# Optimization experiments

Hardware: AMD Instinct MI355X
Metric: run time of the kernel (lower is better)

The kernel has to match this reference:

```python
import jax, jax.numpy as jnp
import numpy as np

B, S, D, H = 16, 2048, 1024, 1024

def setup_inputs() -> dict:
    key = jax.random.key(0)
    k1, k2, k3 = jax.random.split(key, 3)
    X = jax.random.normal(k1, (B, S, D), dtype=jnp.float32)
    W = jax.random.normal(k2, (3 * H, D), dtype=jnp.float32) * (1.0 / np.sqrt(D))
    b = jax.random.normal(k3, (3 * H,), dtype=jnp.float32) * 0.01
    return {"X": X, "W": W, "b": b}

def forget_mult(z, f):
    # z, f: [B, S, H]; h_t = z_t * f_t + (1 - f_t) * h_{t-1}, h_{-1} = 0
    z_t = jnp.moveaxis(z, 1, 0)  # [S, B, H]
    f_t = jnp.moveaxis(f, 1, 0)
    h0 = jnp.zeros(z.shape[::2], dtype=z.dtype)  # [B, H]
    def step(h, zf):
        zt, ft = zf
        h = zt * ft + (1.0 - ft) * h
        return h, h
    _, cs = jax.lax.scan(step, h0, (z_t, f_t))
    return jnp.moveaxis(cs, 0, 1)  # [B, S, H]

def reference(X, W, b):
    # window=1, output_gate=True, batch_first=True, zoneout=0, hidden=None
    Y = jnp.einsum('bsd,ed->bse', X, W) + b  # [B, S, 3H]
    z_gate, f_gate, o_gate = jnp.split(Y, 3, axis=2)
    z_gate = jnp.tanh(z_gate)
    f_gate = jax.nn.sigmoid(f_gate)
    c_gate = forget_mult(z_gate, f_gate)
    output = jax.nn.sigmoid(o_gate) * c_gate
    return output, c_gate[:, -1:]
```

## Files before the change

kernel.cpp:

```cpp
#include <hip/hip_runtime.h>
#include <hip/hip_bf16.h>
#include <hip/hip_fp16.h>


#define BB 16
#define SS 2048
#define DD 1024
#define HH 1024
#define N3 3072
#define CHUNK 64
#define NC (SS/CHUNK)

#define BM 256
#define BN 256
#define BK 64
#define NKT (DD/BK)

typedef _Float16 f16x8 __attribute__((ext_vector_type(8)));
typedef float    f32x4 __attribute__((ext_vector_type(4)));

__device__ __forceinline__ float sigm_f(float x) {
    return 1.0f / (1.0f + __expf(-x));
}
__device__ __forceinline__ float tanh_f(float x) {
    float ax = fabsf(x);
    float e  = __expf(2.0f * ax);
    float r  = 1.0f - 2.0f / (e + 1.0f);
    return copysignf(r, x);
}

__global__ __launch_bounds__(256) void cvt_f32_f16(
    const float* __restrict__ src, __half* __restrict__ dst, int n8)
{
    int i = blockIdx.x * 256 + threadIdx.x;
    if (i >= n8) return;
    const float4* s = (const float4*)src + (size_t)i * 2;
    float4 a = s[0], b = s[1];
    f16x8 v;
    v[0] = (_Float16)a.x; v[1] = (_Float16)a.y; v[2] = (_Float16)a.z; v[3] = (_Float16)a.w;
    v[4] = (_Float16)b.x; v[5] = (_Float16)b.y; v[6] = (_Float16)b.z; v[7] = (_Float16)b.w;
    *((f16x8*)dst + i) = v;
}

__global__ __launch_bounds__(512) void gemm_gates8(
    const __half* __restrict__ Xs,
    const __half* __restrict__ W16,
    const float*  __restrict__ bias,
    __half* __restrict__ G)
{
    __shared__ __half As[2][BM * BK] __attribute__((aligned(16)));
    __shared__ __half Bs[2][BN * BK] __attribute__((aligned(16)));

    const int t   = threadIdx.x;
    const int wid = t >> 6;
    const int l   = t & 63;
    const int m0  = blockIdx.x * BM;
    const int n0  = blockIdx.y * BN;
    const int wr  = wid >> 2;
    const int wc  = wid & 3;
    const int cl  = l & 15;
    const int kg  = l >> 4;
    const int cs  = cl & 7;

    f32x4 acc[8][4];
    #pragma unroll
    for (int m = 0; m < 8; ++m)
        #pragma unroll
        for (int n = 0; n < 4; ++n)
            acc[m][n] = f32x4{0.f, 0.f, 0.f, 0.f};

    const int srow = wid * 8 + (l >> 3);
    const int scol = (((l & 7) ^ ((l >> 3) & 7)) * 8);
    const __half* Xb = Xs  + (size_t)(m0 + srow) * DD + scol;
    const __half* Wb = W16 + (size_t)(n0 + srow) * DD + scol;

#define ISSUE_A(slot, j, kt) \
    __builtin_amdgcn_global_load_lds( \
        (const __attribute__((address_space(1))) void*)(Xb + (size_t)(j) * 64 * DD + (kt) * BK), \
        (__attribute__((address_space(3))) void*)(&As[slot][(j) * 4096 + wid * 512]), 16, 0, 0)
#define ISSUE_B(slot, j, kt) \
    __builtin_amdgcn_global_load_lds( \
        (const __attribute__((address_space(1))) void*)(Wb + (size_t)(j) * 64 * DD + (kt) * BK), \
        (__attribute__((address_space(3))) void*)(&Bs[slot][(j) * 4096 + wid * 512]), 16, 0, 0)

#define READ_A(rh) \
    _Pragma("unroll") \
    for (int i = 0; i < 4; ++i) \
        _Pragma("unroll") \
        for (int kh = 0; kh < 2; ++kh) \
            a[i][kh] = *(const f16x8*)(Ab + ((wr * 128 + ((rh) * 4 + i) * 16 + cl) * BK \
                                             + (((kh * 4 + kg) ^ cs) * 8)))
#define READ_B(bd, ch) \
    _Pragma("unroll") \
    for (int j = 0; j < 2; ++j) \
        _Pragma("unroll") \
        for (int kh = 0; kh < 2; ++kh) \
            bd[j][kh] = *(const f16x8*)(Bb + ((wc * 64 + ((ch) * 2 + j) * 16 + cl) * BK \
                                              + (((kh * 4 + kg) ^ cs) * 8)))

#define WAIT_MFMA(rh, ch, bd) \
    asm volatile("s_waitcnt lgkmcnt(0)" ::: "memory"); \
    __builtin_amdgcn_sched_barrier(0); \
    __builtin_amdgcn_s_setprio(1); \
    _Pragma("unroll") \
    for (int kh = 0; kh < 2; ++kh) \
        _Pragma("unroll") \
        for (int i = 0; i < 4; ++i) \
            _Pragma("unroll") \
            for (int j = 0; j < 2; ++j) \
                acc[(rh) * 4 + i][(ch) * 2 + j] = __builtin_amdgcn_mfma_f32_16x16x32_f16( \
                    a[i][kh], bd[j][kh], acc[(rh) * 4 + i][(ch) * 2 + j], 0, 0, 0); \
    __builtin_amdgcn_s_setprio(0)

    ISSUE_A(0, 0, 0); ISSUE_A(0, 1, 0); ISSUE_A(0, 2, 0); ISSUE_A(0, 3, 0);
    ISSUE_B(0, 0, 0); ISSUE_B(0, 1, 0); ISSUE_B(0, 2, 0); ISSUE_B(0, 3, 0);

    for (int kt = 0; kt < NKT; ++kt) {
        const int cur = kt & 1, nxt = cur ^ 1;
        const __half* Ab = As[cur];
        const __half* Bb = Bs[cur];

        if (kt + 1 < NKT) {
            ISSUE_A(nxt, 0, kt + 1); ISSUE_A(nxt, 1, kt + 1);
            ISSUE_A(nxt, 2, kt + 1); ISSUE_A(nxt, 3, kt + 1);
            asm volatile("s_waitcnt vmcnt(4)" ::: "memory");
        } else {
            asm volatile("s_waitcnt vmcnt(0)" ::: "memory");
        }
        __builtin_amdgcn_s_barrier();

        f16x8 a[4][2], b0[2][2], b1[2][2];

        READ_A(0); READ_B(b0, 0);
        WAIT_MFMA(0, 0, b0);

        READ_B(b1, 1);
        if (kt + 1 < NKT) {
            ISSUE_B(nxt, 0, kt + 1); ISSUE_B(nxt, 1, kt + 1);
            ISSUE_B(nxt, 2, kt + 1); ISSUE_B(nxt, 3, kt + 1);
        }
        WAIT_MFMA(0, 1, b1);

        READ_A(1);
        WAIT_MFMA(1, 1, b1);

        WAIT_MFMA(1, 0, b0);

        __builtin_amdgcn_s_barrier();
    }
#undef WAIT_MFMA
#undef READ_A
#undef READ_B
#undef ISSUE_A
#undef ISSUE_B

    __half* sh = &As[0][0];
    const int bcol0 = n0 + wc * 64 + cl;
    float bv[4];
    #pragma unroll
    for (int fc = 0; fc < 4; ++fc) bv[fc] = bias[bcol0 + fc * 16];

    const int row_l = t >> 3;
    const int chunk = t & 7;

    #pragma unroll
    for (int r = 0; r < 4; ++r) {
        if (wr == (r >> 1)) {
            #pragma unroll
            for (int f4 = 0; f4 < 4; ++f4) {
                const int fr = (r & 1) * 4 + f4;
                #pragma unroll
                for (int fc = 0; fc < 4; ++fc) {
                    #pragma unroll
                    for (int i = 0; i < 4; ++i) {
                        sh[(f4 * 16 + kg * 4 + i) * 264 + wc * 64 + fc * 16 + cl] =
                            __float2half(acc[fr][fc][i] + bv[fc]);
                    }
                }
            }
        }
        __builtin_amdgcn_s_barrier();
        {
            const __half* src = sh + row_l * 264 + chunk * 32;
            __half* dst = G + (size_t)(m0 + r * 64 + row_l) * N3 + n0 + chunk * 32;
            #pragma unroll
            for (int k = 0; k < 4; ++k)
                *(f16x8*)(dst + k * 8) = *(const f16x8*)(src + k * 8);
        }
        __builtin_amdgcn_s_barrier();
    }
}

__global__ __launch_bounds__(256) void scan_pass1(
    const __half* __restrict__ G,
    float* __restrict__ Ac, float* __restrict__ Fc)
{
    const int flat = blockIdx.x * 256 + threadIdx.x;
    const int h  = flat & (HH - 1);
    const int c  = (flat >> 10) & (NC - 1);
    const int lb = flat >> 15;

    const __half* g = G + (size_t)(lb * SS + c * CHUNK) * N3 + h;
    float A = 0.f, F = 1.f;
    for (int s = 0; s < CHUNK; ++s) {
        float z = __half2float(g[0]);
        float f = __half2float(g[HH]);
        g += N3;
        float ft = sigm_f(f);
        float fp = 1.f - ft;
        A = tanh_f(z) * ft + fp * A;
        F *= fp;
    }
    Ac[flat] = A;
    Fc[flat] = F;
}

__global__ __launch_bounds__(256) void scan_pass2(
    const float* __restrict__ Ac, const float* __restrict__ Fc,
    float* __restrict__ Hin, float* __restrict__ c_last)
{
    const int flat = blockIdx.x * 256 + threadIdx.x;
    const int lb = flat >> 10;
    const int h  = flat & (HH - 1);
    float hc = 0.f;
    for (int c = 0; c < NC; ++c) {
        const size_t idx = (size_t)(lb * NC + c) * HH + h;
        Hin[idx] = hc;
        hc = Ac[idx] + Fc[idx] * hc;
    }
    c_last[flat] = hc;
}

__global__ __launch_bounds__(256) void scan_pass3(
    const __half* __restrict__ G, const float* __restrict__ Hin,
    float* __restrict__ out)
{
    const int flat = blockIdx.x * 256 + threadIdx.x;
    const int h  = flat & (HH - 1);
    const int c  = (flat >> 10) & (NC - 1);
    const int lb = flat >> 15;

    const __half* g = G + (size_t)(lb * SS + c * CHUNK) * N3 + h;
    float* o = out + (size_t)(lb * SS + c * CHUNK) * HH + h;
    float hc = Hin[flat];
    for (int s = 0; s < CHUNK; ++s) {
        float z  = __half2float(g[0]);
        float f  = __half2float(g[HH]);
        float og = __half2float(g[2 * HH]);
        g += N3;
        float ft = sigm_f(f);
        hc = tanh_f(z) * ft + (1.f - ft) * hc;
        *o = hc * sigm_f(og);
        o += HH;
    }
}

extern "C" void kernel_launch(void* const* d_in, const int* in_sizes, int n_in,
                              void* d_out, int out_size, void* d_ws, size_t ws_size,
                              hipStream_t stream) {
    const float* X    = (const float*)d_in[0];
    const float* W    = (const float*)d_in[1];
    const float* bias = (const float*)d_in[2];
    for (int i = 0; i < n_in && i < 3; ++i) {
        if      (in_sizes[i] == BB * SS * DD) X    = (const float*)d_in[i];
        else if (in_sizes[i] == N3 * DD)      W    = (const float*)d_in[i];
        else if (in_sizes[i] == N3)           bias = (const float*)d_in[i];
    }
    float* out = (float*)d_out;
    float* c_last_base = out + (size_t)BB * SS * HH;

    const size_t w16_b   = (size_t)N3 * DD * sizeof(__half);
    const size_t per_b_x = (size_t)SS * DD * sizeof(__half);
    const size_t per_b_g = (size_t)SS * N3 * sizeof(__half);
    const size_t per_b_s = (size_t)NC * HH * sizeof(float) * 3;
    int nb = 1;
    for (int cand = BB; cand >= 1; --cand) {
        if (w16_b + (size_t)cand * (per_b_x + per_b_g + per_b_s) <= ws_size) {
            nb = cand; break;
        }
    }
    if (nb > 8) nb = 8;

    __half* W16 = (__half*)d_ws;
    __half* X16 = (__half*)((char*)W16 + w16_b);
    __half* G   = (__half*)((char*)X16 + (size_t)nb * per_b_x);
    float*  Ac  = (float*)((char*)G + (size_t)nb * per_b_g);
    float*  Fc  = Ac + (size_t)nb * NC * HH;
    float*  Hin = Fc + (size_t)nb * NC * HH;

    {
        const int n8 = (N3 * DD) / 8;
        cvt_f32_f16<<<(n8 + 255) / 256, 256, 0, stream>>>(W, W16, n8);
    }

    for (int b0 = 0; b0 < BB; b0 += nb) {
        const int bs = (b0 + nb <= BB) ? nb : (BB - b0);

        const int n8x = (bs * SS * DD) / 8;
        cvt_f32_f16<<<(n8x + 255) / 256, 256, 0, stream>>>(
            X + (size_t)b0 * SS * DD, X16, n8x);

        dim3 gg(bs * (SS / BM), N3 / BN);
        gemm_gates8<<<gg, 512, 0, stream>>>(X16, W16, bias, G);

        scan_pass1<<<(bs * NC * HH) / 256, 256, 0, stream>>>(G, Ac, Fc);
        scan_pass2<<<(bs * HH) / 256, 256, 0, stream>>>(Ac, Fc, Hin,
                                                        c_last_base + (size_t)b0 * HH);
        scan_pass3<<<(bs * NC * HH) / 256, 256, 0, stream>>>(G, Hin,
                                                             out + (size_t)b0 * SS * HH);
    }
}
```

Before: 414.9 us.

## Overlap LDS fragment reads with MFMA using partial lgkmcnt waits and early B prefetch

Issues all next-tile global-to-LDS loads for both A and B at the top of each k-iteration and waits with vmcnt(8). It also separates A fragments into two register sets so LDS reads for later quadrants can be in flight while earlier MFMA quadrants run, using partial lgkmcnt waits and barriers between quadrants. The aim is to hide LDS read latency behind matrix-core work. The cost is more live registers and extra workgroup barriers per iteration, which could lower occupancy or add stalls.

```diff
diff --git a/kernel.cpp b/kernel.cpp
--- a/kernel.cpp
+++ b/kernel.cpp
@@ -83,13 +83,13 @@
         (const __attribute__((address_space(1))) void*)(Wb + (size_t)(j) * 64 * DD + (kt) * BK), \
         (__attribute__((address_space(3))) void*)(&Bs[slot][(j) * 4096 + wid * 512]), 16, 0, 0)
 
-#define READ_A(rh) \
+#define READ_A(ad, rh) \
     _Pragma("unroll") \
     for (int i = 0; i < 4; ++i) \
         _Pragma("unroll") \
         for (int kh = 0; kh < 2; ++kh) \
-            a[i][kh] = *(const f16x8*)(Ab + ((wr * 128 + ((rh) * 4 + i) * 16 + cl) * BK \
-                                             + (((kh * 4 + kg) ^ cs) * 8)))
+            ad[i][kh] = *(const f16x8*)(Ab + ((wr * 128 + ((rh) * 4 + i) * 16 + cl) * BK \
+                                              + (((kh * 4 + kg) ^ cs) * 8)))
 #define READ_B(bd, ch) \
     _Pragma("unroll") \
     for (int j = 0; j < 2; ++j) \
@@ -98,8 +98,7 @@
             bd[j][kh] = *(const f16x8*)(Bb + ((wc * 64 + ((ch) * 2 + j) * 16 + cl) * BK \
                                               + (((kh * 4 + kg) ^ cs) * 8)))
 
-#define WAIT_MFMA(rh, ch, bd) \
-    asm volatile("s_waitcnt lgkmcnt(0)" ::: "memory"); \
+#define MFMA_Q(ad, rh, ch, bd) \
     __builtin_amdgcn_sched_barrier(0); \
     __builtin_amdgcn_s_setprio(1); \
     _Pragma("unroll") \
@@ -109,8 +108,9 @@
             _Pragma("unroll") \
             for (int j = 0; j < 2; ++j) \
                 acc[(rh) * 4 + i][(ch) * 2 + j] = __builtin_amdgcn_mfma_f32_16x16x32_f16( \
-                    a[i][kh], bd[j][kh], acc[(rh) * 4 + i][(ch) * 2 + j], 0, 0, 0); \
-    __builtin_amdgcn_s_setprio(0)
+                    ad[i][kh], bd[j][kh], acc[(rh) * 4 + i][(ch) * 2 + j], 0, 0, 0); \
+    __builtin_amdgcn_s_setprio(0); \
+    __builtin_amdgcn_sched_barrier(0)
 
     ISSUE_A(0, 0, 0); ISSUE_A(0, 1, 0); ISSUE_A(0, 2, 0); ISSUE_A(0, 3, 0);
     ISSUE_B(0, 0, 0); ISSUE_B(0, 1, 0); ISSUE_B(0, 2, 0); ISSUE_B(0, 3, 0);
@@ -123,32 +123,34 @@
         if (kt + 1 < NKT) {
             ISSUE_A(nxt, 0, kt + 1); ISSUE_A(nxt, 1, kt + 1);
             ISSUE_A(nxt, 2, kt + 1); ISSUE_A(nxt, 3, kt + 1);
-            asm volatile("s_waitcnt vmcnt(4)" ::: "memory");
+            ISSUE_B(nxt, 0, kt + 1); ISSUE_B(nxt, 1, kt + 1);
+            ISSUE_B(nxt, 2, kt + 1); ISSUE_B(nxt, 3, kt + 1);
+            asm volatile("s_waitcnt vmcnt(8)" ::: "memory");
         } else {
             asm volatile("s_waitcnt vmcnt(0)" ::: "memory");
         }
         __builtin_amdgcn_s_barrier();
 
-        f16x8 a[4][2], b0[2][2], b1[2][2];
-
-        READ_A(0); READ_B(b0, 0);
-        WAIT_MFMA(0, 0, b0);
-
-        READ_B(b1, 1);
-        if (kt + 1 < NKT) {
-            ISSUE_B(nxt, 0, kt + 1); ISSUE_B(nxt, 1, kt + 1);
-            ISSUE_B(nxt, 2, kt + 1); ISSUE_B(nxt, 3, kt + 1);
-        }
-        WAIT_MFMA(0, 1, b1);
-
-        READ_A(1);
-        WAIT_MFMA(1, 1, b1);
-
-        WAIT_MFMA(1, 0, b0);
-
-        __builtin_amdgcn_s_barrier();
-    }
-#undef WAIT_MFMA
+        f16x8 a0[4][2], a1[4][2], b0[2][2], b1[2][2];
+
+        READ_A(a0, 0); READ_B(b0, 0); READ_B(b1, 1);
+        asm volatile("s_waitcnt lgkmcnt(4)" ::: "memory");
+        MFMA_Q(a0, 0, 0, b0);
+        __builtin_amdgcn_s_barrier();
+
+        READ_A(a1, 1);
+        asm volatile("s_waitcnt lgkmcnt(8)" ::: "memory");
+        MFMA_Q(a0, 0, 1, b1);
+        __builtin_amdgcn_s_barrier();
+
+        asm volatile("s_waitcnt lgkmcnt(0)" ::: "memory");
+        MFMA_Q(a1, 1, 1, b1);
+        __builtin_amdgcn_s_barrier();
+
+        MFMA_Q(a1, 1, 0, b0);
+        __builtin_amdgcn_s_barrier();
+    }
+#undef MFMA_Q
 #undef READ_A
 #undef READ_B
 #undef ISSUE_A
```

Result: slower. 427.0 us (+2.9%).
